# Kernel tuning notes

Hardware: AMD Instinct MI355X
Metric: run time of the kernel (lower is better)

## Reference

```python
import jax, jax.numpy as jnp
import numpy as np

N = 4096      # sentences in document
K = 32        # clusters (args.k)
D = 256       # input_dim
H = 128       # hidden_dim
P_SAL = 0.5   # args.percent_sal


def setup_inputs() -> dict:
    key = jax.random.key(0)
    ks = jax.random.split(key, 12)
    s = 1.0 / np.sqrt(H)
    inp = {
        "sent_gae_embeds": jax.random.normal(ks[0], (N, D), jnp.float32),
        "labels": jax.random.randint(ks[1], (N,), 0, K),
        # GRU layer 0 (torch gate order r,z,n)
        "W_ih0": jax.random.uniform(ks[2], (3 * H, D), jnp.float32, -s, s),
        "W_hh0": jax.random.uniform(ks[3], (3 * H, H), jnp.float32, -s, s),
        "b_ih0": jax.random.uniform(ks[4], (3 * H,), jnp.float32, -s, s),
        "b_hh0": jax.random.uniform(ks[5], (3 * H,), jnp.float32, -s, s),
        # GRU layer 1
        "W_ih1": jax.random.uniform(ks[6], (3 * H, H), jnp.float32, -s, s),
        "W_hh1": jax.random.uniform(ks[7], (3 * H, H), jnp.float32, -s, s),
        "b_ih1": jax.random.uniform(ks[8], (3 * H,), jnp.float32, -s, s),
        "b_hh1": jax.random.uniform(ks[9], (3 * H,), jnp.float32, -s, s),
        # weight-normed linear: W = g * v / ||v|| (norm over input dim)
        "lin_v": jax.random.normal(ks[10], (1, D + H), jnp.float32) * 0.05,
        "lin_g": jnp.ones((1, 1), jnp.float32),
        "lin_b": jnp.zeros((1,), jnp.float32),
    }
    return inp


def _gru_layer(x, W_ih, W_hh, b_ih, b_hh):
    # x: [T, B, Din] -> outputs [T, B, H]
    xw = jnp.einsum("tbd,gd->tbg", x, W_ih) + b_ih  # precompute input gates

    def step(h, xw_t):
        hw = h @ W_hh.T + b_hh
        r = jax.nn.sigmoid(xw_t[:, :H] + hw[:, :H])
        z = jax.nn.sigmoid(xw_t[:, H:2 * H] + hw[:, H:2 * H])
        n = jnp.tanh(xw_t[:, 2 * H:] + r * hw[:, 2 * H:])
        h_new = (1.0 - z) * n + z * h
        return h_new, h_new

    h0 = jnp.zeros((x.shape[1], H), x.dtype)
    _, outs = jax.lax.scan(step, h0, xw)
    return outs


def reference(sent_gae_embeds, labels, W_ih0, W_hh0, b_ih0, b_hh0,
              W_ih1, W_hh1, b_ih1, b_hh1, lin_v, lin_g, lin_b):
    # --- cluster gather: position of each sentence within its cluster ---
    onehot = jax.nn.one_hot(labels, K, dtype=jnp.int32)          # [N, K]
    pos = jnp.cumsum(onehot, axis=0)[jnp.arange(N), labels] - 1  # [N]
    lengths = onehot.sum(axis=0)                                 # [K]

    # padded per-cluster sequences: [T=N, B=K, D]
    padded = jnp.zeros((N, K, D), sent_gae_embeds.dtype).at[pos, labels].set(sent_gae_embeds)

    # --- 2-layer GRU over each cluster sequence ---
    h1 = _gru_layer(padded, W_ih0, W_hh0, b_ih0, b_hh0)
    h2 = _gru_layer(h1, W_ih1, W_hh1, b_ih1, b_hh1)
    len_c = jnp.maximum(lengths, 1)  # empty cluster -> length-1 zero sequence
    cluster_embeds = h2[len_c - 1, jnp.arange(K)]  # [K, H]

    # --- scatter cluster embeds back onto sentences (sent detached as in torch) ---
    sent_d = jax.lax.stop_gradient(sent_gae_embeds)
    final_embeds = jnp.concatenate([sent_d, cluster_embeds[labels]], axis=-1)  # [N, D+H]

    # weight-normed linear + tanh
    Wn = lin_g * lin_v / jnp.linalg.norm(lin_v, axis=1, keepdims=True)
    scores = jnp.tanh(final_embeds @ Wn.T + lin_b)[:, 0]  # [N]

    # salience: per-cluster segment-sum normalization
    clu_scores = jax.ops.segment_sum(scores, labels, num_segments=K)
    sal_scores = scores / clu_scores[labels]

    # position scores: max(0.5, exp(-(i+1)/n**(1/3)))
    inv = np.float32(1.0 / (N ** (1.0 / 3.0)))
    pos_scores = jnp.maximum(0.5, jnp.exp(-(jnp.arange(N, dtype=jnp.float32) + 1.0) * inv))

    return P_SAL * sal_scores + (1.0 - P_SAL) * pos_scores
```

## Files before the change

### kernel.cpp

```cpp
#include <hip/hip_runtime.h>
#include <cmath>

#define NN 4096
#define KK 32
#define DD 256
#define HH 128
#define G3 384
#define CH 16
#define RH 136

typedef __attribute__((ext_vector_type(8))) _Float16 h8;
typedef __attribute__((ext_vector_type(4))) float f32x4;

__device__ __forceinline__ void bar_lds() {
  asm volatile("s_waitcnt lgkmcnt(0)" ::: "memory");
  __builtin_amdgcn_s_barrier();
}

__global__ __launch_bounds__(256) void prep_k(
    const int* __restrict__ labels, const float* __restrict__ lin_v,
    const float* __restrict__ lin_g,
    const float* __restrict__ Whh0, const float* __restrict__ Wih1,
    const float* __restrict__ Whh1,
    const float* __restrict__ sent, const float* __restrict__ W_ih0,
    const float* __restrict__ b_ih0,
    int* __restrict__ order, int* __restrict__ len, float* __restrict__ scale,
    _Float16* __restrict__ P, float* __restrict__ xw,
    float* __restrict__ sdot) {
  const int blk = blockIdx.x;
  const int t = threadIdx.x;
  if (blk < 72) {
    const int gid = blk * 256 + t;
    const int lane = gid & 63;
    const int kt = (gid >> 6) & 3;
    const int nt = (gid >> 8) % 24;
    const int mat = (gid >> 8) / 24;
    const float* W = (mat == 0) ? Whh0 : (mat == 1 ? Wih1 : Whh1);
    const int n = nt * 16 + (lane & 15);
    const int kbase = kt * 32 + (lane >> 4) * 8;
    _Float16* dst = P + (size_t)gid * 8;
#pragma unroll
    for (int j = 0; j < 8; ++j) dst[j] = (_Float16)W[(size_t)n * HH + kbase + j];
    return;
  }
  if (blk < 80) {
    const int wv = t >> 6, lane = t & 63;
    const int c = (blk - 72) * 4 + wv;
    int count = 0;
    for (int base = 0; base < NN; base += 64) {
      const int i = base + lane;
      const bool f = (labels[i] == c);
      const unsigned long long m = __ballot(f);
      if (f) order[c * NN + count + __popcll(m & ((1ull << lane) - 1ull))] = i;
      count += __popcll(m);
    }
    if (lane == 0) len[c] = count;
    return;
  }
  if (blk == 80) {
    if (t < 64) {
      float s = 0.f;
      for (int j = t; j < G3; j += 64) { const float v = lin_v[j]; s += v * v; }
      for (int off = 32; off; off >>= 1) s += __shfl_down(s, off);
      if (t == 0) scale[0] = lin_g[0] / sqrtf(s);
    }
    return;
  }
  if (blk >= 273) {
    const int b = blk - 273;
    const int wv = t >> 6, lane = t & 63;
    const float4 vv = *(const float4*)(lin_v + lane * 4);
    const int r0 = b * 64 + wv * 16;
    for (int rr = 0; rr < 16; ++rr) {
      const int r = r0 + rr;
      const float4 a = *(const float4*)(sent + (size_t)r * DD + lane * 4);
      float d = a.x * vv.x + a.y * vv.y + a.z * vv.z + a.w * vv.w;
      for (int off = 32; off; off >>= 1) d += __shfl_down(d, off);
      if (lane == 0) sdot[r] = d;
    }
    return;
  }
  __shared__ float Xs[16][132];
  __shared__ float Ws[16][68];
  const int g = blk - 81;
  const int i0 = (g & 31) * 128;
  const int g0 = (g >> 5) * 64;
  const int it = t & 15;
  const int gt = t >> 4;
  const int u0 = t * 2, u1 = t * 2 + 1;
  const int ra0 = u0 >> 2, ca0 = u0 & 3;
  const int ra1 = u1 >> 2, ca1 = u1 & 3;
  const int rw_ = t >> 2, cw_ = t & 3;
  float acc[8][4] = {};
  float4 x0, x1, w0;
  x0 = *(const float4*)(sent + (size_t)(i0 + ra0) * DD + ca0 * 4);
  x1 = *(const float4*)(sent + (size_t)(i0 + ra1) * DD + ca1 * 4);
  w0 = *(const float4*)(W_ih0 + (size_t)(g0 + rw_) * DD + cw_ * 4);
  for (int k0 = 0; k0 < DD; k0 += 16) {
    Xs[ca0 * 4 + 0][ra0] = x0.x; Xs[ca0 * 4 + 1][ra0] = x0.y;
    Xs[ca0 * 4 + 2][ra0] = x0.z; Xs[ca0 * 4 + 3][ra0] = x0.w;
    Xs[ca1 * 4 + 0][ra1] = x1.x; Xs[ca1 * 4 + 1][ra1] = x1.y;
    Xs[ca1 * 4 + 2][ra1] = x1.z; Xs[ca1 * 4 + 3][ra1] = x1.w;
    Ws[cw_ * 4 + 0][rw_] = w0.x; Ws[cw_ * 4 + 1][rw_] = w0.y;
    Ws[cw_ * 4 + 2][rw_] = w0.z; Ws[cw_ * 4 + 3][rw_] = w0.w;
    bar_lds();
    if (k0 + 16 < DD) {
      const int kn = k0 + 16;
      x0 = *(const float4*)(sent + (size_t)(i0 + ra0) * DD + kn + ca0 * 4);
      x1 = *(const float4*)(sent + (size_t)(i0 + ra1) * DD + kn + ca1 * 4);
      w0 = *(const float4*)(W_ih0 + (size_t)(g0 + rw_) * DD + kn + cw_ * 4);
    }
#pragma unroll
    for (int k = 0; k < 16; ++k) {
      float a[8], b[4];
#pragma unroll
      for (int x = 0; x < 8; ++x) a[x] = Xs[k][it * 8 + x];
#pragma unroll
      for (int y = 0; y < 4; ++y) b[y] = Ws[k][gt * 4 + y];
#pragma unroll
      for (int x = 0; x < 8; ++x)
#pragma unroll
        for (int y = 0; y < 4; ++y)
          acc[x][y] += a[x] * b[y];
    }
    bar_lds();
  }
  const float4 bs = *(const float4*)(b_ih0 + g0 + gt * 4);
#pragma unroll
  for (int x = 0; x < 8; ++x) {
    const int gi = i0 + it * 8 + x;
    float4 o;
    o.x = acc[x][0] + bs.x; o.y = acc[x][1] + bs.y;
    o.z = acc[x][2] + bs.z; o.w = acc[x][3] + bs.w;
    *(float4*)(xw + (size_t)gi * G3 + g0 + gt * 4) = o;
  }
}

__global__ __launch_bounds__(768) void gru_fused_k(
    const float* __restrict__ xw0,
    const _Float16* __restrict__ pack,
    const float* __restrict__ b_hh0, const float* __restrict__ b_ih0,
    const float* __restrict__ b_ih1, const float* __restrict__ b_hh1,
    const int* __restrict__ len, const int* __restrict__ order,
    const float* __restrict__ sdot,
    const float* __restrict__ lin_v, const float* __restrict__ scale,
    const float* __restrict__ lin_b, float* __restrict__ out) {
  const int c = blockIdx.x;
  const int t = threadIdx.x;
  const int wv = t >> 6, lane = t & 63;
  const int group = wv >> 2;
  const int v = wv & 3;
  h8 B[6][4];
  {
    const _Float16* mp = pack + (size_t)group * (24 * 4 * 64 * 8);
#pragma unroll
    for (int i = 0; i < 6; ++i) {
      const int nt = (i >> 1) * 8 + 2 * v + (i & 1);
#pragma unroll
      for (int kt = 0; kt < 4; ++kt)
        B[i][kt] = *(const h8*)(mp + ((size_t)(nt * 4 + kt) * 64 + lane) * 8);
    }
  }
  const int L = len[c];
  const int Lr = (L > 0) ? L : 1;
  const bool use_bih0 = (L == 0);
  const int u0 = t / 96, f0 = t - u0 * 96;
  const int u1 = (t + 768) / 96, f1 = (t + 768) - u1 * 96;
  const float4* const xsrc = (const float4*)xw0;
  __shared__ __align__(16) float xwbuf[2 * CH * G3];
  __shared__ __align__(16) _Float16 ring[16][2 * RH];
  __shared__ __align__(16) _Float16 hp2[2][2][HH];
  __shared__ float xw1buf[2][8][G3];
  __shared__ float ce_s[HH];
  __shared__ float vbuf[HH];
  __shared__ float sc_s[2048];
  __shared__ float sc_red;
  {
    _Float16* rp = &ring[0][0];
    for (int u = t; u < 16 * 2 * RH; u += 768) rp[u] = (_Float16)0.f;
  }
  if (t < HH) {
    hp2[0][0][t] = (_Float16)0.f; hp2[0][1][t] = (_Float16)0.f;
    hp2[1][0][t] = (_Float16)0.f; hp2[1][1][t] = (_Float16)0.f;
  }
  if (!use_bih0) {
    float4* dst = (float4*)xwbuf;
    const int r0 = (u0 < L) ? order[c * NN + u0] : 0;
    const int r1 = (u1 < L) ? order[c * NN + u1] : 0;
    dst[t] = xsrc[(size_t)r0 * 96 + f0];
    dst[t + 768] = xsrc[(size_t)r1 * 96 + f1];
  }
  const int tg = 32 * v + (lane & 31);
  float bhr = 0.f, bhz = 0.f, bhn = 0.f;
  float bir = 0.f, biz = 0.f, bin = 0.f;
  float h = 0.f;
  if (lane < 32) {
    if (group == 0) {
      bhr = b_hh0[tg]; bhz = b_hh0[HH + tg]; bhn = b_hh0[2 * HH + tg];
      if (use_bih0) {
        bir = b_ih0[tg]; biz = b_ih0[HH + tg]; bin = b_ih0[2 * HH + tg];
      }
    } else if (group == 2) {
      bhr = b_hh1[tg]; bhz = b_hh1[HH + tg]; bhn = b_hh1[2 * HH + tg];
      bir = b_ih1[tg]; biz = b_ih1[HH + tg]; bin = b_ih1[2 * HH + tg];
    }
  }
  __syncthreads();
  const int q = lane >> 4;
  const int row = lane & 15;
  const int hs = (row == 0 || row == 4) ? 0 : 1;
  const bool hiacc = ((lane >> 4) & 1) != 0;
  float4 pf0 = {0.f, 0.f, 0.f, 0.f}, pf1 = {0.f, 0.f, 0.f, 0.f};
  bool pfv = false;
  for (int it2 = 0; it2 < Lr + 9; ++it2) {
    const int par = it2 & 1;
    const int ph = it2 & (CH - 1);
    if (!use_bih0) {
      if (ph == 6) {
        const int s = (it2 & ~(CH - 1)) + CH;
        if (s < Lr) {
          const int p0 = s + u0;
          const int p1 = s + u1;
          const int r0 = (p0 < L) ? order[c * NN + p0] : 0;
          const int r1 = (p1 < L) ? order[c * NN + p1] : 0;
          pf0 = xsrc[(size_t)r0 * 96 + f0];
          pf1 = xsrc[(size_t)r1 * 96 + f1];
          pfv = true;
        }
      } else if (ph == 14 && pfv) {
        const int s = (it2 & ~(CH - 1)) + CH;
        float4* dst = (float4*)(xwbuf + (((s >> 4) & 1) ? CH * G3 : 0));
        dst[t] = pf0;
        dst[t + 768] = pf1;
        pfv = false;
      }
    }
    if (group == 0) {
      if (it2 < Lr) {
        float xr = bir, xz = biz, xn = bin;
        if (!use_bih0 && lane < 32) {
          const float* xrow = xwbuf + ((it2 >> 4) & 1) * (CH * G3)
                                    + (it2 & (CH - 1)) * G3;
          xr = xrow[tg]; xz = xrow[HH + tg]; xn = xrow[2 * HH + tg];
        }
        const _Float16* abse = &ring[(it2 - 1) & 15][hs * RH];
        h8 A[4];
#pragma unroll
        for (int kt = 0; kt < 4; ++kt)
          A[kt] = *(const h8*)(abse + kt * 32 + q * 8);
        f32x4 a0[6];
#pragma unroll
        for (int i = 0; i < 6; ++i) {
          f32x4 a = {0.f, 0.f, 0.f, 0.f};
#pragma unroll
          for (int kt = 0; kt < 4; ++kt)
            a = __builtin_amdgcn_mfma_f32_16x16x32_f16(A[kt], B[i][kt], a, 0, 0, 0);
          a0[i] = a;
        }
        if (lane < 32) {
          const float hwrA = a0[0][0] + a0[0][1], hwrB = a0[1][0] + a0[1][1];
          const float hwzA = a0[2][0] + a0[2][1], hwzB = a0[3][0] + a0[3][1];
          const float hwnA = a0[4][0] + a0[4][1], hwnB = a0[5][0] + a0[5][1];
          const float hwr = hiacc ? hwrB : hwrA;
          const float hwz = hiacc ? hwzB : hwzA;
          const float hwn = hiacc ? hwnB : hwnA;
          const float r = 1.f / (1.f + __expf(-(xr + bhr + hwr)));
          const float z = 1.f / (1.f + __expf(-(xz + bhz + hwz)));
          float tgt = xn + r * (bhn + hwn);
          tgt = fminf(fmaxf(tgt, -15.f), 15.f);
          const float e = __expf(2.f * tgt);
          const float n = (e - 1.f) / (e + 1.f);
          h = (1.f - z) * n + z * h;
          const _Float16 hi = (_Float16)h;
          _Float16* rs = &ring[it2 & 15][0];
          rs[tg] = hi;  rs[RH + tg] = (_Float16)(h - (float)hi);
        }
      }
    } else if (group == 1) {
      if (it2 >= 8 && (it2 & 7) == 0 && it2 - 8 < Lr) {
        const int c8 = it2 - 8;
        const int m = lane & 15;
        const int s = m >> 1, half = m & 1;
        const _Float16* abse = &ring[(c8 + s) & 15][half * RH];
        h8 A[4];
#pragma unroll
        for (int kt = 0; kt < 4; ++kt)
          A[kt] = *(const h8*)(abse + kt * 32 + q * 8);
        const int cbuf = (c8 >> 3) & 1;
        float* xo0 = &xw1buf[cbuf][2 * q][0];
        float* xo1 = &xw1buf[cbuf][2 * q + 1][0];
#pragma unroll
        for (int i = 0; i < 6; ++i) {
          f32x4 a = {0.f, 0.f, 0.f, 0.f};
#pragma unroll
          for (int kt = 0; kt < 4; ++kt)
            a = __builtin_amdgcn_mfma_f32_16x16x32_f16(A[kt], B[i][kt], a, 0, 0, 0);
          const int nt = (i >> 1) * 8 + 2 * v + (i & 1);
          const int col = nt * 16 + (lane & 15);
          xo0[col] = a[0] + a[1];
          xo1[col] = a[2] + a[3];
        }
      }
    } else {
      if (it2 >= 9) {
        const int j = it2 - 9;
        float xr = 0.f, xz = 0.f, xn = 0.f;
        if (lane < 32) {
          const float* xi = xw1buf[(j >> 3) & 1][j & 7];
          xr = xi[tg] + bir; xz = xi[HH + tg] + biz; xn = xi[2 * HH + tg] + bin;
        }
        const _Float16* hbase = hp2[par][hs];
        h8 A[4];
#pragma unroll
        for (int kt = 0; kt < 4; ++kt)
          A[kt] = *(const h8*)(hbase + kt * 32 + q * 8);
        f32x4 a1[6];
#pragma unroll
        for (int i = 0; i < 6; ++i) {
          f32x4 a = {0.f, 0.f, 0.f, 0.f};
#pragma unroll
          for (int kt = 0; kt < 4; ++kt)
            a = __builtin_amdgcn_mfma_f32_16x16x32_f16(A[kt], B[i][kt], a, 0, 0, 0);
          a1[i] = a;
        }
        if (lane < 32) {
          const float hwrA = a1[0][0] + a1[0][1], hwrB = a1[1][0] + a1[1][1];
          const float hwzA = a1[2][0] + a1[2][1], hwzB = a1[3][0] + a1[3][1];
          const float hwnA = a1[4][0] + a1[4][1], hwnB = a1[5][0] + a1[5][1];
          const float hwr = hiacc ? hwrB : hwrA;
          const float hwz = hiacc ? hwzB : hwzA;
          const float hwn = hiacc ? hwnB : hwnA;
          const float r = 1.f / (1.f + __expf(-(xr + bhr + hwr)));
          const float z = 1.f / (1.f + __expf(-(xz + bhz + hwz)));
          float tgt = xn + r * (bhn + hwn);
          tgt = fminf(fmaxf(tgt, -15.f), 15.f);
          const float e = __expf(2.f * tgt);
          const float n = (e - 1.f) / (e + 1.f);
          h = (1.f - z) * n + z * h;
          const _Float16 hi = (_Float16)h;
          hp2[par ^ 1][0][tg] = hi;
          hp2[par ^ 1][1][tg] = (_Float16)(h - (float)hi);
        }
      }
    }
    bar_lds();
  }
  if (L == 0) return;
  if (group == 2 && lane < 32) ce_s[tg] = h;
  if (t < HH) vbuf[t] = lin_v[DD + t];
  __syncthreads();
  if (wv == 0) {
    float cd = ce_s[lane] * vbuf[lane] + ce_s[64 + lane] * vbuf[64 + lane];
    for (int off = 32; off; off >>= 1) cd += __shfl_down(cd, off);
    if (lane == 0) sc_red = cd;
  }
  __syncthreads();
  const float cedot = sc_red;
  const float sc = scale[0], lb = lin_b[0];
  const int Lc = (L < 2048) ? L : 2048;
  for (int p = t; p < Lc; p += 768) {
    const int i = order[c * NN + p];
    sc_s[p] = tanhf(sc * (sdot[i] + cedot) + lb);
  }
  __syncthreads();
  if (wv == 0) {
    float s = 0.f;
    for (int p = lane; p < Lc; p += 64) s += sc_s[p];
    for (int off = 32; off; off >>= 1) s += __shfl_down(s, off);
    if (lane == 0) sc_red = 1.f / s;
  }
  __syncthreads();
  const float inv = sc_red;
  for (int p = t; p < Lc; p += 768) {
    const int i = order[c * NN + p];
    float ps = __expf(-(float)(i + 1) * 0.0625f);
    ps = fmaxf(0.5f, ps);
    out[i] = 0.5f * (sc_s[p] * inv) + 0.5f * ps;
  }
}

extern "C" void kernel_launch(void* const* d_in, const int* in_sizes, int n_in,
                              void* d_out, int out_size, void* d_ws, size_t ws_size,
                              hipStream_t stream) {
  const float* sent   = (const float*)d_in[0];
  const int*   labels = (const int*)d_in[1];
  const float* W_ih0  = (const float*)d_in[2];
  const float* W_hh0  = (const float*)d_in[3];
  const float* b_ih0  = (const float*)d_in[4];
  const float* b_hh0  = (const float*)d_in[5];
  const float* W_ih1  = (const float*)d_in[6];
  const float* W_hh1  = (const float*)d_in[7];
  const float* b_ih1  = (const float*)d_in[8];
  const float* b_hh1  = (const float*)d_in[9];
  const float* lin_v  = (const float*)d_in[10];
  const float* lin_g  = (const float*)d_in[11];
  const float* lin_b  = (const float*)d_in[12];
  float* out = (float*)d_out;

  char* ws = (char*)d_ws;
  size_t off = 0;
  auto alloc = [&](size_t bytes) -> void* {
    void* p = ws + off;
    off = (off + bytes + 255) & ~(size_t)255;
    return p;
  };
  int*   order  = (int*)  alloc((size_t)KK * NN * sizeof(int));
  int*   len    = (int*)  alloc(KK * sizeof(int));
  float* scale  = (float*)alloc(sizeof(float));
  _Float16* pack = (_Float16*)alloc((size_t)18432 * 8 * sizeof(_Float16));
  float* xw     = (float*)alloc((size_t)NN * G3 * sizeof(float));
  float* sdot   = (float*)alloc((size_t)NN * sizeof(float));
  (void)ws_size; (void)in_sizes; (void)n_in; (void)out_size;

  prep_k<<<dim3(337), dim3(256), 0, stream>>>(
      labels, lin_v, lin_g, W_hh0, W_ih1, W_hh1,
      sent, W_ih0, b_ih0, order, len, scale, pack, xw, sdot);
  gru_fused_k<<<dim3(KK), dim3(768), 0, stream>>>(
      xw, pack, b_hh0, b_ih0, b_ih1, b_hh1, len, order,
      sdot, lin_v, scale, lin_b, out);
}
```

Measured before the change: 235.7 us.

## Offload xw0 prefetch to idle wavegroup and shorten recurrent MFMA chains

The global prefetch of precomputed layer-0 input gates moves from all 12 waves into the mostly idle group-1 waves (6 float4 loads each), so the latency-critical recurrent groups no longer issue global loads. Each 4-deep MFMA accumulation chain is split into two independent accumulators that are summed at the end, which shortens the dependent-MFMA latency on the serial per-step path. The recurrent groups raise wave priority with s_setprio, and the ring/h LDS loads are issued before the xw reads. The cost is more registers in group 1 and extra vector adds per tile.

Result: slower. 276.7 us (+17.4%).

```diff
diff --git a/kernel.cpp b/kernel.cpp
--- a/kernel.cpp
+++ b/kernel.cpp
@@ -164,9 +164,16 @@
   const int L = len[c];
   const int Lr = (L > 0) ? L : 1;
   const bool use_bih0 = (L == 0);
+  const float4* const xsrc = (const float4*)xw0;
   const int u0 = t / 96, f0 = t - u0 * 96;
   const int u1 = (t + 768) / 96, f1 = (t + 768) - u1 * 96;
-  const float4* const xsrc = (const float4*)xw0;
+  const int tid1 = (wv - 4) * 64 + lane;
+  int su[6], sf[6];
+#pragma unroll
+  for (int j = 0; j < 6; ++j) {
+    const int e = tid1 + j * 256;
+    su[j] = e / 96; sf[j] = e - su[j] * 96;
+  }
   __shared__ __align__(16) float xwbuf[2 * CH * G3];
   __shared__ __align__(16) _Float16 ring[16][2 * RH];
   __shared__ __align__(16) _Float16 hp2[2][2][HH];
@@ -210,52 +217,36 @@
   const int row = lane & 15;
   const int hs = (row == 0 || row == 4) ? 0 : 1;
   const bool hiacc = ((lane >> 4) & 1) != 0;
-  float4 pf0 = {0.f, 0.f, 0.f, 0.f}, pf1 = {0.f, 0.f, 0.f, 0.f};
-  bool pfv = false;
+  float4 pf[6];
+#pragma unroll
+  for (int j = 0; j < 6; ++j) pf[j] = {0.f, 0.f, 0.f, 0.f};
   for (int it2 = 0; it2 < Lr + 9; ++it2) {
     const int par = it2 & 1;
     const int ph = it2 & (CH - 1);
-    if (!use_bih0) {
-      if (ph == 6) {
-        const int s = (it2 & ~(CH - 1)) + CH;
-        if (s < Lr) {
-          const int p0 = s + u0;
-          const int p1 = s + u1;
-          const int r0 = (p0 < L) ? order[c * NN + p0] : 0;
-          const int r1 = (p1 < L) ? order[c * NN + p1] : 0;
-          pf0 = xsrc[(size_t)r0 * 96 + f0];
-          pf1 = xsrc[(size_t)r1 * 96 + f1];
-          pfv = true;
-        }
-      } else if (ph == 14 && pfv) {
-        const int s = (it2 & ~(CH - 1)) + CH;
-        float4* dst = (float4*)(xwbuf + (((s >> 4) & 1) ? CH * G3 : 0));
-        dst[t] = pf0;
-        dst[t + 768] = pf1;
-        pfv = false;
-      }
-    }
     if (group == 0) {
       if (it2 < Lr) {
+        __builtin_amdgcn_s_setprio(1);
+        const _Float16* abse = &ring[(it2 - 1) & 15][hs * RH];
+        h8 A[4];
+#pragma unroll
+        for (int kt = 0; kt < 4; ++kt)
+          A[kt] = *(const h8*)(abse + kt * 32 + q * 8);
         float xr = bir, xz = biz, xn = bin;
         if (!use_bih0 && lane < 32) {
           const float* xrow = xwbuf + ((it2 >> 4) & 1) * (CH * G3)
                                     + (it2 & (CH - 1)) * G3;
           xr = xrow[tg]; xz = xrow[HH + tg]; xn = xrow[2 * HH + tg];
         }
-        const _Float16* abse = &ring[(it2 - 1) & 15][hs * RH];
-        h8 A[4];
-#pragma unroll
-        for (int kt = 0; kt < 4; ++kt)
-          A[kt] = *(const h8*)(abse + kt * 32 + q * 8);
         f32x4 a0[6];
 #pragma unroll
         for (int i = 0; i < 6; ++i) {
-          f32x4 a = {0.f, 0.f, 0.f, 0.f};
-#pragma unroll
-          for (int kt = 0; kt < 4; ++kt)
-            a = __builtin_amdgcn_mfma_f32_16x16x32_f16(A[kt], B[i][kt], a, 0, 0, 0);
-          a0[i] = a;
+          f32x4 aE = {0.f, 0.f, 0.f, 0.f};
+          f32x4 aO = {0.f, 0.f, 0.f, 0.f};
+          aE = __builtin_amdgcn_mfma_f32_16x16x32_f16(A[0], B[i][0], aE, 0, 0, 0);
+          aO = __builtin_amdgcn_mfma_f32_16x16x32_f16(A[1], B[i][1], aO, 0, 0, 0);
+          aE = __builtin_amdgcn_mfma_f32_16x16x32_f16(A[2], B[i][2], aE, 0, 0, 0);
+          aO = __builtin_amdgcn_mfma_f32_16x16x32_f16(A[3], B[i][3], aO, 0, 0, 0);
+          a0[i] = aE + aO;
         }
         if (lane < 32) {
           const float hwrA = a0[0][0] + a0[0][1], hwrB = a0[1][0] + a0[1][1];
@@ -275,8 +266,29 @@
           _Float16* rs = &ring[it2 & 15][0];
           rs[tg] = hi;  rs[RH + tg] = (_Float16)(h - (float)hi);
         }
+        __builtin_amdgcn_s_setprio(0);
       }
     } else if (group == 1) {
+      if (!use_bih0) {
+        if (ph == 2) {
+          const int s = (it2 & ~(CH - 1)) + CH;
+          if (s < Lr) {
+#pragma unroll
+            for (int j = 0; j < 6; ++j) {
+              const int p = s + su[j];
+              const int r = (p < L) ? order[c * NN + p] : 0;
+              pf[j] = xsrc[(size_t)r * 96 + sf[j]];
+            }
+          }
+        } else if (ph == 10) {
+          const int s = (it2 & ~(CH - 1)) + CH;
+          if (s < Lr) {
+            float4* dst = (float4*)(xwbuf + (((s >> 4) & 1) ? CH * G3 : 0));
+#pragma unroll
+            for (int j = 0; j < 6; ++j) dst[tid1 + j * 256] = pf[j];
+          }
+        }
+      }
       if (it2 >= 8 && (it2 & 7) == 0 && it2 - 8 < Lr) {
         const int c8 = it2 - 8;
         const int m = lane & 15;
@@ -291,10 +303,13 @@
         float* xo1 = &xw1buf[cbuf][2 * q + 1][0];
 #pragma unroll
         for (int i = 0; i < 6; ++i) {
-          f32x4 a = {0.f, 0.f, 0.f, 0.f};
-#pragma unroll
-          for (int kt = 0; kt < 4; ++kt)
-            a = __builtin_amdgcn_mfma_f32_16x16x32_f16(A[kt], B[i][kt], a, 0, 0, 0);
+          f32x4 aE = {0.f, 0.f, 0.f, 0.f};
+          f32x4 aO = {0.f, 0.f, 0.f, 0.f};
+          aE = __builtin_amdgcn_mfma_f32_16x16x32_f16(A[0], B[i][0], aE, 0, 0, 0);
+          aO = __builtin_amdgcn_mfma_f32_16x16x32_f16(A[1], B[i][1], aO, 0, 0, 0);
+          aE = __builtin_amdgcn_mfma_f32_16x16x32_f16(A[2], B[i][2], aE, 0, 0, 0);
+          aO = __builtin_amdgcn_mfma_f32_16x16x32_f16(A[3], B[i][3], aO, 0, 0, 0);
+          const f32x4 a = aE + aO;
           const int nt = (i >> 1) * 8 + 2 * v + (i & 1);
           const int col = nt * 16 + (lane & 15);
           xo0[col] = a[0] + a[1];
@@ -303,25 +318,28 @@
       }
     } else {
       if (it2 >= 9) {
+        __builtin_amdgcn_s_setprio(1);
         const int j = it2 - 9;
+        const _Float16* hbase = hp2[par][hs];
+        h8 A[4];
+#pragma unroll
+        for (int kt = 0; kt < 4; ++kt)
+          A[kt] = *(const h8*)(hbase + kt * 32 + q * 8);
         float xr = 0.f, xz = 0.f, xn = 0.f;
         if (lane < 32) {
           const float* xi = xw1buf[(j >> 3) & 1][j & 7];
           xr = xi[tg] + bir; xz = xi[HH + tg] + biz; xn = xi[2 * HH + tg] + bin;
         }
-        const _Float16* hbase = hp2[par][hs];
-        h8 A[4];
-#pragma unroll
-        for (int kt = 0; kt < 4; ++kt)
-          A[kt] = *(const h8*)(hbase + kt * 32 + q * 8);
         f32x4 a1[6];
 #pragma unroll
         for (int i = 0; i < 6; ++i) {
-          f32x4 a = {0.f, 0.f, 0.f, 0.f};
-#pragma unroll
-          for (int kt = 0; kt < 4; ++kt)
-            a = __builtin_amdgcn_mfma_f32_16x16x32_f16(A[kt], B[i][kt], a, 0, 0, 0);
-          a1[i] = a;
+          f32x4 aE = {0.f, 0.f, 0.f, 0.f};
+          f32x4 aO = {0.f, 0.f, 0.f, 0.f};
+          aE = __builtin_amdgcn_mfma_f32_16x16x32_f16(A[0], B[i][0], aE, 0, 0, 0);
+          aO = __builtin_amdgcn_mfma_f32_16x16x32_f16(A[1], B[i][1], aO, 0, 0, 0);
+          aE = __builtin_amdgcn_mfma_f32_16x16x32_f16(A[2], B[i][2], aE, 0, 0, 0);
+          aO = __builtin_amdgcn_mfma_f32_16x16x32_f16(A[3], B[i][3], aO, 0, 0, 0);
+          a1[i] = aE + aO;
         }
         if (lane < 32) {
           const float hwrA = a1[0][0] + a1[0][1], hwrB = a1[1][0] + a1[1][1];
@@ -341,6 +359,7 @@
           hp2[par ^ 1][0][tg] = hi;
           hp2[par ^ 1][1][tg] = (_Float16)(h - (float)hi);
         }
+        __builtin_amdgcn_s_setprio(0);
       }
     }
     bar_lds();
```

## Fold layer-1 input projection into recurrence wave groups, drop third group

Applied to the files above, without the earlier changes.

Removes the dedicated wave group that batch-computed the layer-1 input projection (h1·W_ih1) every 8 steps. That work is now split across the two recurrent groups, each doing half of the output tiles with extra W_ih1 fragments held in registers. The block shrinks from 768 to 512 threads and the xw prefetch is redistributed across three slots per thread. This cuts the number of waves taking part in each per-step barrier, but adds register pressure and extra MFMA work on the serial critical-path waves every eighth step.

New measurement: 245.3 us. +4.1%, slower.

```diff
diff --git a/kernel.cpp b/kernel.cpp
--- a/kernel.cpp
+++ b/kernel.cpp
@@ -136,7 +136,7 @@
   }
 }
 
-__global__ __launch_bounds__(768) void gru_fused_k(
+__global__ __launch_bounds__(512) void gru_fused_k(
     const float* __restrict__ xw0,
     const _Float16* __restrict__ pack,
     const float* __restrict__ b_hh0, const float* __restrict__ b_ih0,
@@ -150,22 +150,37 @@
   const int wv = t >> 6, lane = t & 63;
   const int group = wv >> 2;
   const int v = wv & 3;
+  const size_t MSZ = (size_t)24 * 4 * 64 * 8;
   h8 B[6][4];
   {
-    const _Float16* mp = pack + (size_t)group * (24 * 4 * 64 * 8);
+    const _Float16* mp = pack + (group == 0 ? (size_t)0 : 2 * MSZ);
 #pragma unroll
     for (int i = 0; i < 6; ++i) {
       const int nt = (i >> 1) * 8 + 2 * v + (i & 1);
 #pragma unroll
       for (int kt = 0; kt < 4; ++kt)
         B[i][kt] = *(const h8*)(mp + ((size_t)(nt * 4 + kt) * 64 + lane) * 8);
+    }
+  }
+  h8 B2[3][4];
+  {
+    const _Float16* mp1 = pack + 1 * MSZ;
+#pragma unroll
+    for (int ii = 0; ii < 3; ++ii) {
+      const int i = (group == 0) ? ii : 3 + ii;
+      const int nt = (i >> 1) * 8 + 2 * v + (i & 1);
+#pragma unroll
+      for (int kt = 0; kt < 4; ++kt)
+        B2[ii][kt] = *(const h8*)(mp1 + ((size_t)(nt * 4 + kt) * 64 + lane) * 8);
     }
   }
   const int L = len[c];
   const int Lr = (L > 0) ? L : 1;
   const bool use_bih0 = (L == 0);
-  const int u0 = t / 96, f0 = t - u0 * 96;
-  const int u1 = (t + 768) / 96, f1 = (t + 768) - u1 * 96;
+  const int e0 = t, e1 = t + 512, e2 = t + 1024;
+  const int u0 = e0 / 96, f0 = e0 - u0 * 96;
+  const int u1 = e1 / 96, f1 = e1 - u1 * 96;
+  const int u2 = e2 / 96, f2 = e2 - u2 * 96;
   const float4* const xsrc = (const float4*)xw0;
   __shared__ __align__(16) float xwbuf[2 * CH * G3];
   __shared__ __align__(16) _Float16 ring[16][2 * RH];
@@ -177,7 +192,7 @@
   __shared__ float sc_red;
   {
     _Float16* rp = &ring[0][0];
-    for (int u = t; u < 16 * 2 * RH; u += 768) rp[u] = (_Float16)0.f;
+    for (int u = t; u < 16 * 2 * RH; u += 512) rp[u] = (_Float16)0.f;
   }
   if (t < HH) {
     hp2[0][0][t] = (_Float16)0.f; hp2[0][1][t] = (_Float16)0.f;
@@ -187,8 +202,10 @@
     float4* dst = (float4*)xwbuf;
     const int r0 = (u0 < L) ? order[c * NN + u0] : 0;
     const int r1 = (u1 < L) ? order[c * NN + u1] : 0;
-    dst[t] = xsrc[(size_t)r0 * 96 + f0];
-    dst[t + 768] = xsrc[(size_t)r1 * 96 + f1];
+    const int r2 = (u2 < L) ? order[c * NN + u2] : 0;
+    dst[e0] = xsrc[(size_t)r0 * 96 + f0];
+    dst[e1] = xsrc[(size_t)r1 * 96 + f1];
+    dst[e2] = xsrc[(size_t)r2 * 96 + f2];
   }
   const int tg = 32 * v + (lane & 31);
   float bhr = 0.f, bhz = 0.f, bhn = 0.f;
@@ -200,7 +217,7 @@
       if (use_bih0) {
         bir = b_ih0[tg]; biz = b_ih0[HH + tg]; bin = b_ih0[2 * HH + tg];
       }
-    } else if (group == 2) {
+    } else {
       bhr = b_hh1[tg]; bhz = b_hh1[HH + tg]; bhn = b_hh1[2 * HH + tg];
       bir = b_ih1[tg]; biz = b_ih1[HH + tg]; bin = b_ih1[2 * HH + tg];
     }
@@ -210,7 +227,8 @@
   const int row = lane & 15;
   const int hs = (row == 0 || row == 4) ? 0 : 1;
   const bool hiacc = ((lane >> 4) & 1) != 0;
-  float4 pf0 = {0.f, 0.f, 0.f, 0.f}, pf1 = {0.f, 0.f, 0.f, 0.f};
+  float4 pf0 = {0.f, 0.f, 0.f, 0.f}, pf1 = {0.f, 0.f, 0.f, 0.f},
+         pf2 = {0.f, 0.f, 0.f, 0.f};
   bool pfv = false;
   for (int it2 = 0; it2 < Lr + 9; ++it2) {
     const int par = it2 & 1;
@@ -219,19 +237,19 @@
       if (ph == 6) {
         const int s = (it2 & ~(CH - 1)) + CH;
         if (s < Lr) {
-          const int p0 = s + u0;
-          const int p1 = s + u1;
+          const int p0 = s + u0, p1 = s + u1, p2 = s + u2;
           const int r0 = (p0 < L) ? order[c * NN + p0] : 0;
           const int r1 = (p1 < L) ? order[c * NN + p1] : 0;
+          const int r2 = (p2 < L) ? order[c * NN + p2] : 0;
           pf0 = xsrc[(size_t)r0 * 96 + f0];
           pf1 = xsrc[(size_t)r1 * 96 + f1];
+          pf2 = xsrc[(size_t)r2 * 96 + f2];
           pfv = true;
         }
       } else if (ph == 14 && pfv) {
         const int s = (it2 & ~(CH - 1)) + CH;
         float4* dst = (float4*)(xwbuf + (((s >> 4) & 1) ? CH * G3 : 0));
-        dst[t] = pf0;
-        dst[t + 768] = pf1;
+        dst[e0] = pf0; dst[e1] = pf1; dst[e2] = pf2;
         pfv = false;
       }
     }
@@ -276,31 +294,6 @@
           rs[tg] = hi;  rs[RH + tg] = (_Float16)(h - (float)hi);
         }
       }
-    } else if (group == 1) {
-      if (it2 >= 8 && (it2 & 7) == 0 && it2 - 8 < Lr) {
-        const int c8 = it2 - 8;
-        const int m = lane & 15;
-        const int s = m >> 1, half = m & 1;
-        const _Float16* abse = &ring[(c8 + s) & 15][half * RH];
-        h8 A[4];
-#pragma unroll
-        for (int kt = 0; kt < 4; ++kt)
-          A[kt] = *(const h8*)(abse + kt * 32 + q * 8);
-        const int cbuf = (c8 >> 3) & 1;
-        float* xo0 = &xw1buf[cbuf][2 * q][0];
-        float* xo1 = &xw1buf[cbuf][2 * q + 1][0];
-#pragma unroll
-        for (int i = 0; i < 6; ++i) {
-          f32x4 a = {0.f, 0.f, 0.f, 0.f};
-#pragma unroll
-          for (int kt = 0; kt < 4; ++kt)
-            a = __builtin_amdgcn_mfma_f32_16x16x32_f16(A[kt], B[i][kt], a, 0, 0, 0);
-          const int nt = (i >> 1) * 8 + 2 * v + (i & 1);
-          const int col = nt * 16 + (lane & 15);
-          xo0[col] = a[0] + a[1];
-          xo1[col] = a[2] + a[3];
-        }
-      }
     } else {
       if (it2 >= 9) {
         const int j = it2 - 9;
@@ -343,10 +336,35 @@
         }
       }
     }
+    if (it2 >= 8 && (it2 & 7) == 0 && it2 - 8 < Lr) {
+      const int c8 = it2 - 8;
+      const int m = lane & 15;
+      const int s = m >> 1, half = m & 1;
+      const _Float16* abse = &ring[(c8 + s) & 15][half * RH];
+      h8 Ab[4];
+#pragma unroll
+      for (int kt = 0; kt < 4; ++kt)
+        Ab[kt] = *(const h8*)(abse + kt * 32 + q * 8);
+      const int cbuf = (c8 >> 3) & 1;
+      float* xo0 = &xw1buf[cbuf][2 * q][0];
+      float* xo1 = &xw1buf[cbuf][2 * q + 1][0];
+#pragma unroll
+      for (int ii = 0; ii < 3; ++ii) {
+        f32x4 a = {0.f, 0.f, 0.f, 0.f};
+#pragma unroll
+        for (int kt = 0; kt < 4; ++kt)
+          a = __builtin_amdgcn_mfma_f32_16x16x32_f16(Ab[kt], B2[ii][kt], a, 0, 0, 0);
+        const int i = (group == 0) ? ii : 3 + ii;
+        const int nt = (i >> 1) * 8 + 2 * v + (i & 1);
+        const int col = nt * 16 + (lane & 15);
+        xo0[col] = a[0] + a[1];
+        xo1[col] = a[2] + a[3];
+      }
+    }
     bar_lds();
   }
   if (L == 0) return;
-  if (group == 2 && lane < 32) ce_s[tg] = h;
+  if (group == 1 && lane < 32) ce_s[tg] = h;
   if (t < HH) vbuf[t] = lin_v[DD + t];
   __syncthreads();
   if (wv == 0) {
@@ -358,7 +376,7 @@
   const float cedot = sc_red;
   const float sc = scale[0], lb = lin_b[0];
   const int Lc = (L < 2048) ? L : 2048;
-  for (int p = t; p < Lc; p += 768) {
+  for (int p = t; p < Lc; p += 512) {
     const int i = order[c * NN + p];
     sc_s[p] = tanhf(sc * (sdot[i] + cedot) + lb);
   }
@@ -371,7 +389,7 @@
   }
   __syncthreads();
   const float inv = sc_red;
-  for (int p = t; p < Lc; p += 768) {
+  for (int p = t; p < Lc; p += 512) {
     const int i = order[c * NN + p];
     float ps = __expf(-(float)(i + 1) * 0.0625f);
     ps = fmaxf(0.5f, ps);
@@ -415,7 +433,7 @@
   prep_k<<<dim3(337), dim3(256), 0, stream>>>(
       labels, lin_v, lin_g, W_hh0, W_ih1, W_hh1,
       sent, W_ih0, b_ih0, order, len, scale, pack, xw, sdot);
-  gru_fused_k<<<dim3(KK), dim3(768), 0, stream>>>(
+  gru_fused_k<<<dim3(KK), dim3(512), 0, stream>>>(
       xw, pack, b_hh0, b_ih0, b_ih1, b_hh1, len, order,
       sdot, lin_v, scale, lin_b, out);
 }
```
